# Kernel tuning notes

Measured on AMD Instinct MI355X. Metric: run time of the kernel, lower is better.

## Reference

```python
import jax, jax.numpy as jnp
import numpy as np

N = 100000   # nodes
E = 1600000  # edges (avg degree 16)
D_IN = 128
HID = [128, 128]
D_OUT = 1


def _linear_params(key, in_c, out_c):
    k1, k2 = jax.random.split(key)
    s = 1.0 / np.sqrt(in_c)
    w = jax.random.uniform(k1, (out_c, in_c), jnp.float32, -s, s)
    b = jax.random.uniform(k2, (out_c,), jnp.float32, -s, s)
    return w, b


def setup_inputs() -> dict:
    key = jax.random.key(0)
    ks = jax.random.split(key, 16)
    inp = {}
    inp["x"] = jax.random.normal(ks[0], (N, D_IN), jnp.float32)
    inp["edge_index"] = jax.random.randint(ks[1], (2, E), 0, N, jnp.int32)
    # 3 GINConvs: dims (128->128), (128->128), (128->128); each MLP = Linear, ReLU, Linear
    dims = [(D_IN, HID[0]), (HID[0], HID[1]), (HID[1], HID[1])]
    for i, (ic, oc) in enumerate(dims):
        k1, k2 = jax.random.split(ks[2 + i])
        w1, b1 = _linear_params(k1, ic, oc)
        w2, b2 = _linear_params(k2, oc, oc)
        inp[f"c{i}_w1"], inp[f"c{i}_b1"] = w1, b1
        inp[f"c{i}_w2"], inp[f"c{i}_b2"] = w2, b2
        inp[f"c{i}_eps"] = jnp.zeros((), jnp.float32)  # train_eps=True, init 0
    last = HID[-1]
    inp["fc1_w"], inp["fc1_b"] = _linear_params(ks[8], last, last // 2)
    inp["fc2_w"], inp["fc2_b"] = _linear_params(ks[9], last // 2, D_OUT)
    return inp


def reference(x, edge_index,
              c0_w1, c0_b1, c0_w2, c0_b2, c0_eps,
              c1_w1, c1_b1, c1_w2, c1_b2, c1_eps,
              c2_w1, c2_b1, c2_w2, c2_b2, c2_eps,
              fc1_w, fc1_b, fc2_w, fc2_b):
    src, dst = edge_index[0], edge_index[1]  # messages flow src -> dst
    n = x.shape[0]

    def gin_conv(h, w1, b1, w2, b2, eps):
        # sum-aggregate neighbor features: scatter-add h[src] into dst
        agg = jax.ops.segment_sum(h[src], dst, num_segments=n)
        z = (1.0 + eps) * h + agg
        z = jax.nn.relu(z @ w1.T + b1) @ w2.T + b2  # GIN MLP
        return jax.nn.relu(z)  # outer ReLU in GINNet.forward

    h = gin_conv(x, c0_w1, c0_b1, c0_w2, c0_b2, c0_eps)
    h = gin_conv(h, c1_w1, c1_b1, c1_w2, c1_b2, c1_eps)
    h = gin_conv(h, c2_w1, c2_b1, c2_w2, c2_b2, c2_eps)
    h = jax.nn.relu(h @ fc1_w.T + fc1_b)
    return jax.nn.sigmoid(h @ fc2_w.T + fc2_b)
```

## Files before the change

### kernel.cpp

```cpp
#include <hip/hip_runtime.h>
#include <math.h>


using f16   = _Float16;
using f16x4 = __attribute__((ext_vector_type(4))) _Float16;
using f16x8 = __attribute__((ext_vector_type(8))) _Float16;
using f32x4 = __attribute__((ext_vector_type(4))) float;

constexpr int BINBLK = 256;

__device__ inline void glds16(const void* g, void* l) {
    __builtin_amdgcn_global_load_lds(
        (const __attribute__((address_space(1))) void*)g,
        (__attribute__((address_space(3))) void*)l, 16, 0, 0);
}


__global__ __launch_bounds__(512) void bucket_count_kernel(const int* __restrict__ dst,
                                                           int* __restrict__ cntM,
                                                           int E, int nbuck) {
    __shared__ int cnt[512];
    for (int i = threadIdx.x; i < nbuck; i += 512) cnt[i] = 0;
    __syncthreads();
    int chunk = (E + gridDim.x - 1) / gridDim.x;
    int lo = blockIdx.x * chunk, hi = min(lo + chunk, E);
    for (int e = lo + threadIdx.x; e < hi; e += 512)
        atomicAdd(&cnt[dst[e] >> 8], 1);
    __syncthreads();
    for (int i = threadIdx.x; i < nbuck; i += 512)
        cntM[(size_t)i * gridDim.x + blockIdx.x] = cnt[i];
}

__global__ __launch_bounds__(256) void scan_partial(const int* __restrict__ deg,
                                                    int* __restrict__ bsum, int n) {
    __shared__ int red[256];
    int b = blockIdx.x, t = threadIdx.x;
    int base = b * 1024;
    int s = 0;
#pragma unroll
    for (int j = 0; j < 4; ++j) {
        int idx = base + j * 256 + t;
        if (idx < n) s += deg[idx];
    }
    red[t] = s;
    __syncthreads();
    for (int d = 128; d > 0; d >>= 1) {
        if (t < d) red[t] += red[t + d];
        __syncthreads();
    }
    if (t == 0) bsum[b] = red[0];
}

__global__ __launch_bounds__(128) void scan_bsum(const int* __restrict__ bsum,
                                                 int* __restrict__ bbase, int nb,
                                                 int* __restrict__ total_out) {
    __shared__ int s[128];
    int t = threadIdx.x;
    s[t] = (t < nb) ? bsum[t] : 0;
    __syncthreads();
    for (int d = 1; d < 128; d <<= 1) {
        int v = (t >= d) ? s[t - d] : 0;
        __syncthreads();
        s[t] += v;
        __syncthreads();
    }
    bbase[t] = (t > 0) ? s[t - 1] : 0;
    if (t == 127) total_out[0] = s[127];
}

__global__ __launch_bounds__(256) void scan_final(const int* __restrict__ deg,
                                                  const int* __restrict__ bbase,
                                                  int* __restrict__ outA,
                                                  int* __restrict__ outB, int n) {
    __shared__ int red[256];
    int b = blockIdx.x, t = threadIdx.x;
    int base = b * 1024 + t * 4;
    int d0 = 0, d1 = 0, d2 = 0, d3 = 0;
    if (base + 3 < n) {
        int4 v = *(const int4*)&deg[base];
        d0 = v.x; d1 = v.y; d2 = v.z; d3 = v.w;
    } else {
        if (base < n) d0 = deg[base];
        if (base + 1 < n) d1 = deg[base + 1];
        if (base + 2 < n) d2 = deg[base + 2];
    }
    red[t] = d0 + d1 + d2 + d3;
    __syncthreads();
    for (int d = 1; d < 256; d <<= 1) {
        int v = (t >= d) ? red[t - d] : 0;
        __syncthreads();
        red[t] += v;
        __syncthreads();
    }
    int ex = bbase[b] + ((t > 0) ? red[t - 1] : 0);
    int o0 = ex, o1 = ex + d0, o2 = o1 + d1, o3 = o2 + d2;
    if (base + 3 < n) {
        *(int4*)&outA[base] = make_int4(o0, o1, o2, o3);
        *(int4*)&outB[base] = make_int4(o0, o1, o2, o3);
    } else {
        if (base < n) { outA[base] = o0; outB[base] = o0; }
        if (base + 1 < n) { outA[base + 1] = o1; outB[base + 1] = o1; }
        if (base + 2 < n) { outA[base + 2] = o2; outB[base + 2] = o2; }
    }
}

__global__ __launch_bounds__(512) void bin_kernel(const int* __restrict__ src,
                                                  const int* __restrict__ dst,
                                                  const int* __restrict__ baseM,
                                                  int2* __restrict__ stage, int E, int nbuck) {
    __shared__ int cur[512];
    for (int i = threadIdx.x; i < nbuck; i += 512)
        cur[i] = baseM[(size_t)i * gridDim.x + blockIdx.x];
    __syncthreads();
    int chunk = (E + gridDim.x - 1) / gridDim.x;
    int lo = blockIdx.x * chunk, hi = min(lo + chunk, E);
    for (int e = lo + threadIdx.x; e < hi; e += 512) {
        int d = dst[e];
        int p = atomicAdd(&cur[d >> 8], 1);
        stage[p] = make_int2(src[e], d);
    }
}

__global__ __launch_bounds__(256) void csr_kernel(const int2* __restrict__ stage,
                                                  const int* __restrict__ baseM,
                                                  int* __restrict__ offs,
                                                  int* __restrict__ col,
                                                  int E, int N, int nbuck, int binblk) {
    constexpr int CAP = 10240;
    __shared__ int cnt[256];
    __shared__ int sc[256];
    __shared__ int colbuf[CAP];
    int b = blockIdx.x, t = threadIdx.x;
    int base = baseM[(size_t)b * binblk];
    int end = (b + 1 < nbuck) ? baseM[(size_t)(b + 1) * binblk] : E;
    cnt[t] = 0;
    __syncthreads();
    for (int e = base + t; e < end; e += 256)
        atomicAdd(&cnt[stage[e].y & 255], 1);
    __syncthreads();
    int myCnt = cnt[t];
    sc[t] = myCnt;
    __syncthreads();
    for (int d = 1; d < 256; d <<= 1) {
        int u = (t >= d) ? sc[t - d] : 0;
        __syncthreads();
        sc[t] += u;
        __syncthreads();
    }
    int myExcl = sc[t] - myCnt;
    int node = b * 256 + t;
    if (node <= N) offs[node] = base + myExcl;
    cnt[t] = myExcl;
    __syncthreads();
    for (int e = base + t; e < end; e += 256) {
        int2 sd = stage[e];
        int p = atomicAdd(&cnt[sd.y & 255], 1);
        if (p < CAP) colbuf[p] = sd.x;
        else col[base + p] = sd.x;
    }
    __syncthreads();
    int lim = min(end - base, CAP);
    for (int i = t; i < lim; i += 256) col[base + i] = colbuf[i];
}

__global__ void cvt4_kernel(const float* __restrict__ in, f16* __restrict__ out, int nq) {
    int stride = gridDim.x * blockDim.x;
    for (int i = blockIdx.x * blockDim.x + threadIdx.x; i < nq; i += stride) {
        float4 v = *(const float4*)(in + (size_t)i * 4);
        f16x4 o = {(f16)v.x, (f16)v.y, (f16)v.z, (f16)v.w};
        *(f16x4*)(out + (size_t)i * 4) = o;
    }
}

struct CvtPack {
    const float* s[7];
    f16* d[7];
    int nq[7];
};
__global__ void cvt_pack_kernel(CvtPack p) {
    int seg = blockIdx.y;
    int nq = p.nq[seg];
    const float* in = p.s[seg];
    f16* out = p.d[seg];
    int stride = gridDim.x * blockDim.x;
    for (int i = blockIdx.x * blockDim.x + threadIdx.x; i < nq; i += stride) {
        float4 v = *(const float4*)(in + (size_t)i * 4);
        f16x4 o = {(f16)v.x, (f16)v.y, (f16)v.z, (f16)v.w};
        *(f16x4*)(out + (size_t)i * 4) = o;
    }
}

__global__ __launch_bounds__(256) void agg_kernel(const f16* __restrict__ h,
                                                  const int* __restrict__ offs,
                                                  const int* __restrict__ col,
                                                  const float* __restrict__ epsp,
                                                  f16* __restrict__ z, int n) {
    __shared__ int colLDS[2048];
    __shared__ int sOffs[33];
    const int tid = threadIdx.x;
    const int nb = blockIdx.x * 32;
    if (tid < 33) sOffs[tid] = offs[min(nb + tid, n)];
    __syncthreads();
    const int base = sOffs[0];
    const int len = sOffs[32] - base;
    const bool useLds = len <= 2048;
    if (useLds) {
        for (int i = tid; i < len; i += 256)
            colLDS[i] = __builtin_nontemporal_load(&col[base + i]);
    }
    __syncthreads();

    const int grp = tid >> 3;
    const int li = tid & 7;
    const int node = nb + grp;
    const bool valid = node < n;
    const int nd = valid ? node : (n - 1);
    const int lo = sOffs[grp] - base;
    const int hi = valid ? (sOffs[grp + 1] - base) : lo;
    const f16x8* hp = (const f16x8*)h;
    const float e1 = 1.0f + epsp[0];

#pragma unroll
    for (int ph = 0; ph < 2; ++ph) {
        const int co = ph * 8 + li;
        f16x8 self = hp[(size_t)nd * 16 + co];
        float a[8];
#pragma unroll
        for (int c = 0; c < 8; ++c) a[c] = (float)self[c] * e1;
        int e = lo;
        for (; e + 8 <= hi; e += 8) {
            int idx[8];
#pragma unroll
            for (int j = 0; j < 8; ++j)
                idx[j] = useLds ? colLDS[e + j] : col[base + e + j];
            f16x8 v[8];
#pragma unroll
            for (int j = 0; j < 8; ++j) v[j] = hp[(size_t)idx[j] * 16 + co];
#pragma unroll
            for (int j = 0; j < 8; ++j)
#pragma unroll
                for (int c = 0; c < 8; ++c) a[c] += (float)v[j][c];
        }
        if (e + 4 <= hi) {
            int idx[4];
#pragma unroll
            for (int j = 0; j < 4; ++j)
                idx[j] = useLds ? colLDS[e + j] : col[base + e + j];
            f16x8 v[4];
#pragma unroll
            for (int j = 0; j < 4; ++j) v[j] = hp[(size_t)idx[j] * 16 + co];
#pragma unroll
            for (int j = 0; j < 4; ++j)
#pragma unroll
                for (int c = 0; c < 8; ++c) a[c] += (float)v[j][c];
            e += 4;
        }
        for (; e < hi; ++e) {
            int idx = useLds ? colLDS[e] : col[base + e];
            f16x8 v = hp[(size_t)idx * 16 + co];
#pragma unroll
            for (int c = 0; c < 8; ++c) a[c] += (float)v[c];
        }
        if (valid) {
            f16x8 o;
#pragma unroll
            for (int c = 0; c < 8; ++c) o[c] = (f16)a[c];
            __builtin_nontemporal_store(o, (f16x8*)z + (size_t)nd * 16 + co);
        }
    }
}

template <bool LAST>
__global__ __launch_bounds__(256) void conv_mlp_kernel(
    const f16* __restrict__ Z, const f16* __restrict__ W1f,
    const float* __restrict__ b1, const f16* __restrict__ W2f,
    const float* __restrict__ b2, f16* __restrict__ Hout, int M,
    const f16* __restrict__ fc1wf, const float* __restrict__ fc1b,
    const float* __restrict__ fc2w, const float* __restrict__ fc2b,
    float* __restrict__ out) {
    __shared__ __align__(16) f16 As[128 * 128];
    __shared__ __align__(16) f16 Ws[128 * 128];
    __shared__ float Red[LAST ? 128 * 17 : 1];

    const int tid = threadIdx.x;
    const int w = tid >> 6, lane = tid & 63;
    const int frow = lane & 15, kgrp = lane >> 4;
    const int m0 = blockIdx.x * 128;
    const int u = lane & 15, rsub = lane >> 4;

#pragma unroll
    for (int i = 0; i < 8; ++i) {
        int rowbase = (w * 8 + i) * 4;
        int r = rowbase + rsub;
        int gr = m0 + r;
        if (gr >= M) gr = M - 1;
        glds16(Z + (size_t)gr * 128 + ((u ^ (r & 7)) << 3), &As[rowbase * 128]);
    }
#pragma unroll
    for (int i = 0; i < 8; ++i) {
        int rowbase = (w * 8 + i) * 4;
        int r = rowbase + rsub;
        glds16(W1f + (size_t)r * 128 + ((u ^ (r & 7)) << 3), &Ws[rowbase * 128]);
    }
    __syncthreads();

    const int arow0 = w * 32 + frow;
    f32x4 acc[2][8];
#pragma unroll
    for (int mi = 0; mi < 2; ++mi)
#pragma unroll
        for (int nj = 0; nj < 8; ++nj) acc[mi][nj] = (f32x4){0.f, 0.f, 0.f, 0.f};

#pragma unroll
    for (int kk = 0; kk < 4; ++kk) {
        int kb = kk * 4 + kgrp;
        f16x8 a[2], b[8];
#pragma unroll
        for (int mi = 0; mi < 2; ++mi) {
            int r = arow0 + mi * 16;
            a[mi] = *(const f16x8*)&As[r * 128 + ((kb ^ (r & 7)) << 3)];
        }
#pragma unroll
        for (int nj = 0; nj < 8; ++nj) {
            int r = nj * 16 + frow;
            b[nj] = *(const f16x8*)&Ws[r * 128 + ((kb ^ (r & 7)) << 3)];
        }
#pragma unroll
        for (int mi = 0; mi < 2; ++mi)
#pragma unroll
            for (int nj = 0; nj < 8; ++nj)
                acc[mi][nj] = __builtin_amdgcn_mfma_f32_16x16x32_f16(a[mi], b[nj],
                                                                     acc[mi][nj], 0, 0, 0);
    }
    __syncthreads();

#pragma unroll
    for (int i = 0; i < 8; ++i) {
        int rowbase = (w * 8 + i) * 4;
        int r = rowbase + rsub;
        glds16(W2f + (size_t)r * 128 + ((u ^ (r & 7)) << 3), &Ws[rowbase * 128]);
    }
    {
        float bv[8];
#pragma unroll
        for (int nj = 0; nj < 8; ++nj) bv[nj] = b1[nj * 16 + frow];
#pragma unroll
        for (int mi = 0; mi < 2; ++mi)
#pragma unroll
            for (int nj = 0; nj < 8; ++nj) {
                int row0 = w * 32 + mi * 16 + kgrp * 4;
                int c = nj * 16 + frow;
                int cu = c >> 3, cl = c & 7;
#pragma unroll
                for (int r = 0; r < 4; ++r) {
                    int rr = row0 + r;
                    As[rr * 128 + ((cu ^ (rr & 7)) << 3) + cl] =
                        (f16)fmaxf(acc[mi][nj][r] + bv[nj], 0.f);
                }
            }
    }
    __syncthreads();

#pragma unroll
    for (int mi = 0; mi < 2; ++mi)
#pragma unroll
        for (int nj = 0; nj < 8; ++nj) acc[mi][nj] = (f32x4){0.f, 0.f, 0.f, 0.f};
#pragma unroll
    for (int kk = 0; kk < 4; ++kk) {
        int kb = kk * 4 + kgrp;
        f16x8 a[2], b[8];
#pragma unroll
        for (int mi = 0; mi < 2; ++mi) {
            int r = arow0 + mi * 16;
            a[mi] = *(const f16x8*)&As[r * 128 + ((kb ^ (r & 7)) << 3)];
        }
#pragma unroll
        for (int nj = 0; nj < 8; ++nj) {
            int r = nj * 16 + frow;
            b[nj] = *(const f16x8*)&Ws[r * 128 + ((kb ^ (r & 7)) << 3)];
        }
#pragma unroll
        for (int mi = 0; mi < 2; ++mi)
#pragma unroll
            for (int nj = 0; nj < 8; ++nj)
                acc[mi][nj] = __builtin_amdgcn_mfma_f32_16x16x32_f16(a[mi], b[nj],
                                                                     acc[mi][nj], 0, 0, 0);
    }

    float bv2[8];
#pragma unroll
    for (int nj = 0; nj < 8; ++nj) bv2[nj] = b2[nj * 16 + frow];

    if (!LAST) {
        __syncthreads();
#pragma unroll
        for (int mi = 0; mi < 2; ++mi)
#pragma unroll
            for (int nj = 0; nj < 8; ++nj) {
                int row0 = w * 32 + mi * 16 + kgrp * 4;
                int c = nj * 16 + frow;
#pragma unroll
                for (int r = 0; r < 4; ++r)
                    As[(row0 + r) * 128 + c] = (f16)fmaxf(acc[mi][nj][r] + bv2[nj], 0.f);
            }
        __syncthreads();
        for (int idx = tid; idx < 128 * 16; idx += 256) {
            int r = idx >> 4, q = idx & 15;
            int gm = m0 + r;
            if (gm < M)
                *(float4*)(Hout + (size_t)gm * 128 + q * 8) = *(const float4*)&As[r * 128 + q * 8];
        }
    } else {
        __syncthreads();
#pragma unroll
        for (int i = 0; i < 4; ++i) {
            int rowbase = (w * 4 + i) * 4;
            int r = rowbase + rsub;
            glds16(fc1wf + (size_t)r * 128 + ((u ^ (r & 7)) << 3), &Ws[rowbase * 128]);
        }
#pragma unroll
        for (int mi = 0; mi < 2; ++mi)
#pragma unroll
            for (int nj = 0; nj < 8; ++nj) {
                int row0 = w * 32 + mi * 16 + kgrp * 4;
                int c = nj * 16 + frow;
                int cu = c >> 3, cl = c & 7;
#pragma unroll
                for (int r = 0; r < 4; ++r) {
                    int rr = row0 + r;
                    As[rr * 128 + ((cu ^ (rr & 7)) << 3) + cl] =
                        (f16)fmaxf(acc[mi][nj][r] + bv2[nj], 0.f);
                }
            }
        __syncthreads();

        f32x4 acc3[2][4];
#pragma unroll
        for (int mi = 0; mi < 2; ++mi)
#pragma unroll
            for (int nj = 0; nj < 4; ++nj) acc3[mi][nj] = (f32x4){0.f, 0.f, 0.f, 0.f};
#pragma unroll
        for (int kk = 0; kk < 4; ++kk) {
            int kb = kk * 4 + kgrp;
            f16x8 a[2], b[4];
#pragma unroll
            for (int mi = 0; mi < 2; ++mi) {
                int r = arow0 + mi * 16;
                a[mi] = *(const f16x8*)&As[r * 128 + ((kb ^ (r & 7)) << 3)];
            }
#pragma unroll
            for (int nj = 0; nj < 4; ++nj) {
                int r = nj * 16 + frow;
                b[nj] = *(const f16x8*)&Ws[r * 128 + ((kb ^ (r & 7)) << 3)];
            }
#pragma unroll
            for (int mi = 0; mi < 2; ++mi)
#pragma unroll
                for (int nj = 0; nj < 4; ++nj)
                    acc3[mi][nj] = __builtin_amdgcn_mfma_f32_16x16x32_f16(a[mi], b[nj],
                                                                          acc3[mi][nj], 0, 0, 0);
        }
        float bvf[4], f2[4];
#pragma unroll
        for (int nj = 0; nj < 4; ++nj) {
            bvf[nj] = fc1b[nj * 16 + frow];
            f2[nj] = fc2w[nj * 16 + frow];
        }
        float part[2][4];
#pragma unroll
        for (int mi = 0; mi < 2; ++mi)
#pragma unroll
            for (int r = 0; r < 4; ++r) part[mi][r] = 0.f;
#pragma unroll
        for (int mi = 0; mi < 2; ++mi)
#pragma unroll
            for (int nj = 0; nj < 4; ++nj)
#pragma unroll
                for (int r = 0; r < 4; ++r)
                    part[mi][r] += fmaxf(acc3[mi][nj][r] + bvf[nj], 0.f) * f2[nj];
#pragma unroll
        for (int mi = 0; mi < 2; ++mi)
#pragma unroll
            for (int r = 0; r < 4; ++r)
                Red[(w * 32 + mi * 16 + kgrp * 4 + r) * 17 + frow] = part[mi][r];
        __syncthreads();
        if (tid < 128) {
            float s = fc2b[0];
#pragma unroll
            for (int q = 0; q < 16; ++q) s += Red[tid * 17 + q];
            int m = m0 + tid;
            if (m < M) out[m] = 1.f / (1.f + expf(-s));
        }
    }
}

extern "C" void kernel_launch(void* const* d_in, const int* in_sizes, int n_in,
                              void* d_out, int out_size, void* d_ws, size_t ws_size,
                              hipStream_t stream) {
    const float* x = (const float*)d_in[0];
    const int* ei = (const int*)d_in[1];
    const int N = in_sizes[0] / 128;
    const int E = in_sizes[1] / 2;
    const int* srcIdx = ei;
    const int* dstIdx = ei + E;

    const float* w1[3] = {(const float*)d_in[2], (const float*)d_in[7], (const float*)d_in[12]};
    const float* b1[3] = {(const float*)d_in[3], (const float*)d_in[8], (const float*)d_in[13]};
    const float* w2[3] = {(const float*)d_in[4], (const float*)d_in[9], (const float*)d_in[14]};
    const float* b2[3] = {(const float*)d_in[5], (const float*)d_in[10], (const float*)d_in[15]};
    const float* eps[3] = {(const float*)d_in[6], (const float*)d_in[11], (const float*)d_in[16]};
    const float* fc1w = (const float*)d_in[17];
    const float* fc1b = (const float*)d_in[18];
    const float* fc2w = (const float*)d_in[19];
    const float* fc2b = (const float*)d_in[20];

    char* ws = (char*)d_ws;
    size_t p = 0;
    auto carve = [&](size_t bytes) -> char* {
        char* r = ws + p;
        p = (p + bytes + 255) & ~(size_t)255;
        return r;
    };
    const int nbuck = (N + 255) >> 8;
    const int nm = nbuck * BINBLK;
    int* offs = (int*)carve((size_t)(N + 1) * 4);
    int* col = (int*)carve((size_t)E * 4);
    int* cntM = (int*)carve((size_t)nm * 4);
    int* baseM = (int*)carve((size_t)nm * 4);
    int* baseM2 = (int*)carve((size_t)nm * 4);
    int* bsum = (int*)carve(128 * 4);
    int* bbase = (int*)carve(128 * 4);
    int* tot = (int*)carve(4);
    int2* stage = (int2*)carve((size_t)E * 8);
    f16* H0 = (f16*)carve((size_t)N * 128 * 2);
    f16* H1 = (f16*)carve((size_t)N * 128 * 2);
    f16* Z = (f16*)carve((size_t)N * 128 * 2);
    f16* w1f[3], *w2f[3];
    for (int i = 0; i < 3; ++i) {
        w1f[i] = (f16*)carve(128 * 128 * 2);
        w2f[i] = (f16*)carve(128 * 128 * 2);
    }
    f16* fc1wf = (f16*)carve(64 * 128 * 2);
    (void)ws_size;

    const int SB2 = (nm + 1023) / 1024;
    bucket_count_kernel<<<BINBLK, 512, 0, stream>>>(dstIdx, cntM, E, nbuck);
    scan_partial<<<SB2, 256, 0, stream>>>(cntM, bsum, nm);
    scan_bsum<<<1, 128, 0, stream>>>(bsum, bbase, SB2, tot);
    scan_final<<<SB2, 256, 0, stream>>>(cntM, bbase, baseM, baseM2, nm);
    bin_kernel<<<BINBLK, 512, 0, stream>>>(srcIdx, dstIdx, baseM, stage, E, nbuck);
    csr_kernel<<<nbuck, 256, 0, stream>>>(stage, baseM, offs, col, E, N, nbuck, BINBLK);

    cvt4_kernel<<<2048, 256, 0, stream>>>(x, H0, N * 128 / 4);
    CvtPack cp;
    for (int i = 0; i < 3; ++i) {
        cp.s[i] = w1[i];     cp.d[i] = w1f[i];     cp.nq[i] = 128 * 128 / 4;
        cp.s[3 + i] = w2[i]; cp.d[3 + i] = w2f[i]; cp.nq[3 + i] = 128 * 128 / 4;
    }
    cp.s[6] = fc1w; cp.d[6] = fc1wf; cp.nq[6] = 64 * 128 / 4;
    cvt_pack_kernel<<<dim3(16, 7), 256, 0, stream>>>(cp);

    const int aggGrid = (N + 31) / 32;
    const int gemmGrid = (N + 127) / 128;

    agg_kernel<<<aggGrid, 256, 0, stream>>>(H0, offs, col, eps[0], Z, N);
    conv_mlp_kernel<false><<<gemmGrid, 256, 0, stream>>>(
        Z, w1f[0], b1[0], w2f[0], b2[0], H1, N, nullptr, nullptr, nullptr, nullptr, nullptr);
    agg_kernel<<<aggGrid, 256, 0, stream>>>(H1, offs, col, eps[1], Z, N);
    conv_mlp_kernel<false><<<gemmGrid, 256, 0, stream>>>(
        Z, w1f[1], b1[1], w2f[1], b2[1], H0, N, nullptr, nullptr, nullptr, nullptr, nullptr);
    agg_kernel<<<aggGrid, 256, 0, stream>>>(H0, offs, col, eps[2], Z, N);
    conv_mlp_kernel<true><<<gemmGrid, 256, 0, stream>>>(
        Z, w1f[2], b1[2], w2f[2], b2[2], nullptr, N, fc1wf, fc1b, fc2w, fc2b, (float*)d_out);
}
```

Baseline: 289.3 us.

## Pack staged edges into one int and double-buffer gather batches in aggregation

The binning stage now stores each edge as a single 32-bit word (source shifted left by 8, low byte holding the destination's index within its bucket), which halves the staging buffer traffic. The unused duplicate scan output baseM2 is removed. In the aggregation kernel, the 8-wide neighbour gather loop is software-pipelined with two register buffers, so the next batch's loads are issued before the previous batch is accumulated. The packing relies on source indices fitting in 24 bits, and the double buffer raises register pressure in the gather kernel.

```diff
diff --git a/kernel.cpp b/kernel.cpp
--- a/kernel.cpp
+++ b/kernel.cpp
@@ -70,8 +70,7 @@
 
 __global__ __launch_bounds__(256) void scan_final(const int* __restrict__ deg,
                                                   const int* __restrict__ bbase,
-                                                  int* __restrict__ outA,
-                                                  int* __restrict__ outB, int n) {
+                                                  int* __restrict__ outA, int n) {
     __shared__ int red[256];
     int b = blockIdx.x, t = threadIdx.x;
     int base = b * 1024 + t * 4;
@@ -96,18 +95,17 @@
     int o0 = ex, o1 = ex + d0, o2 = o1 + d1, o3 = o2 + d2;
     if (base + 3 < n) {
         *(int4*)&outA[base] = make_int4(o0, o1, o2, o3);
-        *(int4*)&outB[base] = make_int4(o0, o1, o2, o3);
     } else {
-        if (base < n) { outA[base] = o0; outB[base] = o0; }
-        if (base + 1 < n) { outA[base + 1] = o1; outB[base + 1] = o1; }
-        if (base + 2 < n) { outA[base + 2] = o2; outB[base + 2] = o2; }
+        if (base < n) outA[base] = o0;
+        if (base + 1 < n) outA[base + 1] = o1;
+        if (base + 2 < n) outA[base + 2] = o2;
     }
 }
 
 __global__ __launch_bounds__(512) void bin_kernel(const int* __restrict__ src,
                                                   const int* __restrict__ dst,
                                                   const int* __restrict__ baseM,
-                                                  int2* __restrict__ stage, int E, int nbuck) {
+                                                  int* __restrict__ stage, int E, int nbuck) {
     __shared__ int cur[512];
     for (int i = threadIdx.x; i < nbuck; i += 512)
         cur[i] = baseM[(size_t)i * gridDim.x + blockIdx.x];
@@ -117,11 +115,11 @@
     for (int e = lo + threadIdx.x; e < hi; e += 512) {
         int d = dst[e];
         int p = atomicAdd(&cur[d >> 8], 1);
-        stage[p] = make_int2(src[e], d);
-    }
-}
-
-__global__ __launch_bounds__(256) void csr_kernel(const int2* __restrict__ stage,
+        stage[p] = (src[e] << 8) | (d & 255);
+    }
+}
+
+__global__ __launch_bounds__(256) void csr_kernel(const int* __restrict__ stage,
                                                   const int* __restrict__ baseM,
                                                   int* __restrict__ offs,
                                                   int* __restrict__ col,
@@ -136,7 +134,7 @@
     cnt[t] = 0;
     __syncthreads();
     for (int e = base + t; e < end; e += 256)
-        atomicAdd(&cnt[stage[e].y & 255], 1);
+        atomicAdd(&cnt[stage[e] & 255], 1);
     __syncthreads();
     int myCnt = cnt[t];
     sc[t] = myCnt;
@@ -153,10 +151,10 @@
     cnt[t] = myExcl;
     __syncthreads();
     for (int e = base + t; e < end; e += 256) {
-        int2 sd = stage[e];
-        int p = atomicAdd(&cnt[sd.y & 255], 1);
-        if (p < CAP) colbuf[p] = sd.x;
-        else col[base + p] = sd.x;
+        int sd = stage[e];
+        int p = atomicAdd(&cnt[sd & 255], 1);
+        if (p < CAP) colbuf[p] = sd >> 8;
+        else col[base + p] = sd >> 8;
     }
     __syncthreads();
     int lim = min(end - base, CAP);
@@ -227,19 +225,71 @@
         float a[8];
 #pragma unroll
         for (int c = 0; c < 8; ++c) a[c] = (float)self[c] * e1;
+
         int e = lo;
-        for (; e + 8 <= hi; e += 8) {
-            int idx[8];
-#pragma unroll
-            for (int j = 0; j < 8; ++j)
-                idx[j] = useLds ? colLDS[e + j] : col[base + e + j];
-            f16x8 v[8];
-#pragma unroll
-            for (int j = 0; j < 8; ++j) v[j] = hp[(size_t)idx[j] * 16 + co];
-#pragma unroll
-            for (int j = 0; j < 8; ++j)
-#pragma unroll
-                for (int c = 0; c < 8; ++c) a[c] += (float)v[j][c];
+        const int nbatch = (hi - lo) >> 3;
+        if (nbatch > 0) {
+            f16x8 v[8], w[8];
+            {
+                int idx[8];
+#pragma unroll
+                for (int j = 0; j < 8; ++j)
+                    idx[j] = useLds ? colLDS[e + j] : col[base + e + j];
+#pragma unroll
+                for (int j = 0; j < 8; ++j) v[j] = hp[(size_t)idx[j] * 16 + co];
+            }
+            int b = 1;
+            for (; b + 1 < nbatch; b += 2) {
+                int e1i = lo + b * 8;
+                {
+                    int idx[8];
+#pragma unroll
+                    for (int j = 0; j < 8; ++j)
+                        idx[j] = useLds ? colLDS[e1i + j] : col[base + e1i + j];
+#pragma unroll
+                    for (int j = 0; j < 8; ++j) w[j] = hp[(size_t)idx[j] * 16 + co];
+                }
+#pragma unroll
+                for (int j = 0; j < 8; ++j)
+#pragma unroll
+                    for (int c = 0; c < 8; ++c) a[c] += (float)v[j][c];
+                int e2i = lo + (b + 1) * 8;
+                {
+                    int idx[8];
+#pragma unroll
+                    for (int j = 0; j < 8; ++j)
+                        idx[j] = useLds ? colLDS[e2i + j] : col[base + e2i + j];
+#pragma unroll
+                    for (int j = 0; j < 8; ++j) v[j] = hp[(size_t)idx[j] * 16 + co];
+                }
+#pragma unroll
+                for (int j = 0; j < 8; ++j)
+#pragma unroll
+                    for (int c = 0; c < 8; ++c) a[c] += (float)w[j][c];
+            }
+            if (b < nbatch) {
+                int e1i = lo + b * 8;
+                int idx[8];
+#pragma unroll
+                for (int j = 0; j < 8; ++j)
+                    idx[j] = useLds ? colLDS[e1i + j] : col[base + e1i + j];
+#pragma unroll
+                for (int j = 0; j < 8; ++j) w[j] = hp[(size_t)idx[j] * 16 + co];
+#pragma unroll
+                for (int j = 0; j < 8; ++j)
+#pragma unroll
+                    for (int c = 0; c < 8; ++c) a[c] += (float)v[j][c];
+#pragma unroll
+                for (int j = 0; j < 8; ++j)
+#pragma unroll
+                    for (int c = 0; c < 8; ++c) a[c] += (float)w[j][c];
+            } else {
+#pragma unroll
+                for (int j = 0; j < 8; ++j)
+#pragma unroll
+                    for (int c = 0; c < 8; ++c) a[c] += (float)v[j][c];
+            }
+            e = lo + nbatch * 8;
         }
         if (e + 4 <= hi) {
             int idx[4];
@@ -527,11 +577,10 @@
     int* col = (int*)carve((size_t)E * 4);
     int* cntM = (int*)carve((size_t)nm * 4);
     int* baseM = (int*)carve((size_t)nm * 4);
-    int* baseM2 = (int*)carve((size_t)nm * 4);
     int* bsum = (int*)carve(128 * 4);
     int* bbase = (int*)carve(128 * 4);
     int* tot = (int*)carve(4);
-    int2* stage = (int2*)carve((size_t)E * 8);
+    int* stage = (int*)carve((size_t)E * 4);
     f16* H0 = (f16*)carve((size_t)N * 128 * 2);
     f16* H1 = (f16*)carve((size_t)N * 128 * 2);
     f16* Z = (f16*)carve((size_t)N * 128 * 2);
@@ -547,7 +596,7 @@
     bucket_count_kernel<<<BINBLK, 512, 0, stream>>>(dstIdx, cntM, E, nbuck);
     scan_partial<<<SB2, 256, 0, stream>>>(cntM, bsum, nm);
     scan_bsum<<<1, 128, 0, stream>>>(bsum, bbase, SB2, tot);
-    scan_final<<<SB2, 256, 0, stream>>>(cntM, bbase, baseM, baseM2, nm);
+    scan_final<<<SB2, 256, 0, stream>>>(cntM, bbase, baseM, nm);
     bin_kernel<<<BINBLK, 512, 0, stream>>>(srcIdx, dstIdx, baseM, stage, E, nbuck);
     csr_kernel<<<nbuck, 256, 0, stream>>>(stage, baseM, offs, col, E, N, nbuck, BINBLK);
 
```

Result: slower. 314.5 us (+8.7%).
